# Kernel optimization log

Hardware: AMD Instinct MI355X
Metric: run time of the kernel (lower is better)

The kernel has to match this reference:

```python
import jax, jax.numpy as jnp
import numpy as np
from jax import lax

N, HW = 64, 240
C0, C1, C2, C3 = 3, 32, 64, 128
HEAD = 1280


def _conv(x, w, stride, pad):
    return lax.conv_general_dilated(
        x, w, (stride, stride), [(pad, pad), (pad, pad)],
        dimension_numbers=("NCHW", "OIHW", "NCHW"))


def _cbr(x, w, alpha, beta, stride, pad, do_relu=True):
    # conv2d with pre-folded BN: y = conv(x,w)*alpha + beta, then ReLU
    y = _conv(x, w, stride, pad)
    y = y * alpha[None, :, None, None] + beta[None, :, None, None]
    return jnp.maximum(y, 0.0) if do_relu else y


def setup_inputs() -> dict:
    key = jax.random.key(0)
    ks = jax.random.split(key, 13)
    f32 = jnp.float32
    inp = {
        "x": jax.random.normal(ks[0], (N, C0, HW, HW), dtype=f32),
        # stem 3x3 s2: 3 -> 32
        "w_stem": jax.random.normal(ks[1], (C1, C0, 3, 3), dtype=f32) * 0.1,
        "a_stem": jax.random.uniform(ks[2], (C1,), dtype=f32, minval=0.5, maxval=1.5),
        "b_stem": jax.random.normal(ks[3], (C1,), dtype=f32) * 0.1,
        # mid 3x3 s2: 32 -> 64
        "w1": jax.random.normal(ks[4], (C2, C1, 3, 3), dtype=f32) * 0.05,
        "a1": jax.random.uniform(ks[5], (C2,), dtype=f32, minval=0.5, maxval=1.5),
        "b1": jax.random.normal(ks[6], (C2,), dtype=f32) * 0.1,
        # pointwise 1x1 s1: 64 -> 128
        "w2": jax.random.normal(ks[7], (C3, C2, 1, 1), dtype=f32) * 0.05,
        "a2": jax.random.uniform(ks[8], (C3,), dtype=f32, minval=0.5, maxval=1.5),
        "b2": jax.random.normal(ks[9], (C3,), dtype=f32) * 0.1,
        # head: GAP + GEMV (w2d [Cout, Cin]) + BN-fold + ReLU
        "w_head": jax.random.normal(ks[10], (HEAD, C3), dtype=f32) * 0.05,
        "a_head": jax.random.uniform(ks[11], (HEAD,), dtype=f32, minval=0.5, maxval=1.5),
        "b_head": jax.random.normal(ks[12], (HEAD,), dtype=f32) * 0.1,
    }
    return inp


def reference(x, w_stem, a_stem, b_stem, w1, a1, b1, w2, a2, b2,
              w_head, a_head, b_head):
    h = _cbr(x, w_stem, a_stem, b_stem, stride=2, pad=1)   # [N,32,120,120]
    h = _cbr(h, w1, a1, b1, stride=2, pad=1)               # [N,64,60,60]
    h = _cbr(h, w2, a2, b2, stride=1, pad=0)               # [N,128,60,60]
    # head: global average pool + GEMV + folded-BN affine + ReLU
    gap = h.mean(axis=(2, 3))                              # [N,128]
    out = jnp.einsum("nc,oc->no", gap, w_head)             # [N,1280]
    out = out * a_head[None, :] + b_head[None, :]
    return jnp.maximum(out, 0.0)
```

## Files before the change

### kernel.cpp

```cpp
#include <hip/hip_runtime.h>

#define N_    64
#define HW_   240
#define H1_   120
#define H2_   60
#define C0_   3
#define C1_   32
#define C2_   64
#define C3_   128
#define HEAD_ 1280

typedef unsigned short US;
typedef short bf16x8 __attribute__((ext_vector_type(8)));
typedef float f32x16 __attribute__((ext_vector_type(16)));

__device__ __forceinline__ US f2bf(float f) {
  union { float f; unsigned u; } v; v.f = f;
  unsigned r = v.u + 0x7FFF + ((v.u >> 16) & 1);
  return (US)(r >> 16);
}

#define H1Q_ROW 3968
#define H1Q_PL  1984

__device__ __forceinline__ void gld_lds16(const void* g, void* l) {
  __builtin_amdgcn_global_load_lds(
      (const __attribute__((address_space(1))) unsigned int*)g,
      (__attribute__((address_space(3))) unsigned int*)l, 16, 0, 0);
}

#define ZCHN   368
#define ZTOT   (64 * ZCHN * 4)
__global__ __launch_bounds__(256) void k0_prep(
    const float* __restrict__ w1, const float* __restrict__ w2,
    const float* __restrict__ w0,
    US* __restrict__ h1q, US* __restrict__ wt1, US* __restrict__ wt2,
    US* __restrict__ wt0, float* __restrict__ gap) {
  int gid = blockIdx.x * 256 + threadIdx.x;
  if (gid < ZTOT) {
    int c = gid >> 2, q = gid & 3;
    int n = c / ZCHN, cc = c % ZCHN;
    long off; int y;
    if (cc < 124)      { y = 0;   off = (long)cc * 32; }
    else if (cc < 248) { y = 121; off = (long)(cc - 124) * 32; }
    else               { y = cc - 247; off = H1Q_PL; }
    uint4 z; z.x = z.y = z.z = z.w = 0u;
    *(uint4*)(h1q + ((long)(n * 122 + y)) * H1Q_ROW + off + q * 8) = z;
  } else if (gid < ZTOT + 18432) {
    int e = gid - ZTOT;
    int oc = e / 288, ic = (e / 9) % 32, ky = (e / 3) % 3, kx = e % 3;
    wt1[((ky * 3 + kx) * 64 + oc) * 32 + ic] = f2bf(w1[e]);
  } else if (gid < ZTOT + 18432 + 8192) {
    int e = gid - (ZTOT + 18432);
    wt2[e] = f2bf(w2[e]);
  } else if (gid < ZTOT + 18432 + 8192 + 1024) {
    int e = gid - (ZTOT + 18432 + 8192);
    int oc = e >> 5, k = e & 31;
    wt0[e] = (k < 27) ? f2bf(w0[oc * 27 + k]) : (US)0;
  } else if (gid < ZTOT + 18432 + 8192 + 1024 + 8192) {
    gap[gid - (ZTOT + 18432 + 8192 + 1024)] = 0.f;
  }
}

#define XSW 248
__global__ __launch_bounds__(256) void k1_mfma(
    const float* __restrict__ x, const US* __restrict__ wt0,
    const float* __restrict__ alpha, const float* __restrict__ beta,
    US* __restrict__ h1q) {
  __shared__ __align__(16) float xs[3 * 3 * XSW];
  __shared__ US ot[128 * 32];
  int y = blockIdx.x, n = blockIdx.y;
  int iy0 = 2 * y - 1;
  const float* xn = x + (long)n * C0_ * HW_ * HW_;
  int t = threadIdx.x, w = t >> 6, l = t & 63;

  if (t < 18) {
    int seg = t >> 1, end = t & 1;
    float4 z; z.x = z.y = z.z = z.w = 0.f;
    *(float4*)(xs + seg * XSW + (end ? 244 : 0)) = z;
  }
  if (y == 0) {
    float4 z; z.x = z.y = z.z = z.w = 0.f;
    for (int e = t; e < 180; e += 256) {
      int m = e % 60, icz = e / 60;
      *(float4*)(xs + (icz * 3) * XSW + 4 + 4 * m) = z;
    }
  }
  __syncthreads();

  for (int sgi = w; sgi < 9; sgi += 4) {
    int ic = sgi / 3, r = sgi - (sgi / 3) * 3;
    int iy = iy0 + r;
    if (iy >= 0 && l < 60)
      gld_lds16((const char*)(xn + (long)ic * HW_ * HW_ + (long)iy * HW_) +
                    l * 16,
                (char*)(xs + sgi * XSW + 4) + l * 16);
  }
  __syncthreads();

  int wv = w;
  int lane31 = l & 31, half = l >> 5;
  int ox = wv * 32 + lane31;
  int oxc = ox < H1_ ? ox : (H1_ - 1);

  float fa[16];
#pragma unroll
  for (int m = 0; m < 2; m++)
#pragma unroll
    for (int j = 0; j < 8; j++) {
      int k = m * 16 + half * 8 + j;
      float v = 0.f;
      if (k < 27) {
        int ic = k / 9, rem = k - ic * 9;
        int ky = rem / 3, kx = rem - ky * 3;
        v = xs[(ic * 3 + ky) * XSW + 3 + 2 * oxc + kx];
      }
      fa[m * 8 + j] = v;
    }
  bf16x8 a0, a1;
#pragma unroll
  for (int j = 0; j < 8; j++) {
    a0[j] = (short)f2bf(fa[j]);
    a1[j] = (short)f2bf(fa[8 + j]);
  }
  const US* wb = wt0 + lane31 * 32 + half * 8;
  bf16x8 b0 = *(const bf16x8*)(wb);
  bf16x8 b1 = *(const bf16x8*)(wb + 16);

  f32x16 acc;
#pragma unroll
  for (int i = 0; i < 16; i++) acc[i] = 0.f;
  acc = __builtin_amdgcn_mfma_f32_32x32x16_bf16(a0, b0, acc, 0, 0, 0);
  acc = __builtin_amdgcn_mfma_f32_32x32x16_bf16(a1, b1, acc, 0, 0, 0);

  int oc = lane31;
  float al = alpha[oc], be = beta[oc];
#pragma unroll
  for (int r = 0; r < 16; r++) {
    int row = (r & 3) + 8 * (r >> 2) + 4 * half;
    float v = fmaxf(fmaf(acc[r], al, be), 0.f);
    ot[(wv * 32 + row) * 32 + oc] = f2bf(v);
  }
  __syncthreads();

  long rowb = ((long)(n * 122 + y + 1)) * H1Q_ROW;
  for (int u = t; u < 480; u += 256) {
    int px = u >> 2, q = u & 3;
    int pl = px & 1;
    int m = (px + 1) >> 1;
    long addr = rowb + (pl ? H1Q_PL : 0) + (long)m * 32 + q * 8;
    *(uint4*)(h1q + addr) = *(const uint4*)(ot + px * 32 + q * 8);
  }
}

#define TS 72
__global__ __launch_bounds__(256, 2) void k2_fused(
    const US* __restrict__ h1q, const US* __restrict__ wt1,
    const US* __restrict__ wt2,
    const float* __restrict__ a1, const float* __restrict__ b1,
    const float* __restrict__ a2, const float* __restrict__ b2,
    float* __restrict__ gap) {
  __shared__ __align__(16) US st[6 * 4096];
  __shared__ __align__(16) US tile[64 * TS];
  int t = threadIdx.x, w = t >> 6, l = t & 63;
  int lane31 = l & 31, half = l >> 5;

  int n = 8 * blockIdx.x + (blockIdx.y & 7);
  int bxr = blockIdx.y >> 3;
  int ny = bxr < 4 ? 8 : 7;
  int y0 = bxr < 4 ? bxr * 8 : 32 + (bxr - 4) * 7;

  const char* nb = (const char*)(h1q + (long)(n * 122) * H1Q_ROW);

  int wm = w & 1, wn = w >> 1;
  int oc = wn * 32 + lane31;
  int pt = w & 1, og = w >> 1;
  bf16x8 wA[9][2];
#pragma unroll
  for (int kk = 0; kk < 9; kk++)
#pragma unroll
    for (int c = 0; c < 2; c++)
      wA[kk][c] = *(const bf16x8*)(wt1 + (kk * 64 + oc) * 32 + half * 8 + c * 16);
  bf16x8 wB[2][4];
  float al2[2], be2[2];
#pragma unroll
  for (int nt = 0; nt < 2; nt++) {
    int oc2 = (og * 2 + nt) * 32 + lane31;
#pragma unroll
    for (int c = 0; c < 4; c++)
      wB[nt][c] = *(const bf16x8*)(wt2 + oc2 * 64 + half * 8 + c * 16);
    al2[nt] = a2[oc2]; be2[nt] = b2[oc2];
  }
  float al1 = a1[oc], be1 = b1[oc];

  int px = wm * 32 + lane31;
  int xx = px < 60 ? px : 59;
  int abase = xx * 32 + half * 8;
  int usofs[3][2];
#pragma unroll
  for (int kx = 0; kx < 3; kx++)
#pragma unroll
    for (int c = 0; c < 2; c++) {
      int uo = (kx == 1 ? 0 : (kx == 0 ? 1984 : 2016)) + abase + c * 16;
      usofs[kx][c] = uo ^ (((uo >> 6) & 7) << 3);
    }

#pragma unroll
  for (int i = 0; i < 6; i++) {
    int c = i * 256 + t;
    int rw = c >> 9;
    int b = (c & 511) * 16;
    int sb = b ^ (((b >> 7) & 7) << 4);
    int r = 2 * y0 + rw;
    gld_lds16(nb + (long)r * 7936 + sb, (char*)st + (r % 6) * 8192 + b);
  }
  __syncthreads();

  for (int iy = 0; iy < ny; iy++) {
    int y = y0 + iy;
    if (iy + 1 < ny) {
#pragma unroll
      for (int i = 0; i < 4; i++) {
        int c = i * 256 + t;
        int rw = c >> 9;
        int b = (c & 511) * 16;
        int sb = b ^ (((b >> 7) & 7) << 4);
        int r = 2 * y + 3 + rw;
        gld_lds16(nb + (long)r * 7936 + sb,
                  (char*)st + (r % 6) * 8192 + b);
      }
    }

    f32x16 acc;
#pragma unroll
    for (int i = 0; i < 16; i++) acc[i] = 0.f;
#pragma unroll
    for (int ky = 0; ky < 3; ky++) {
      int r = 2 * y + ky;
      int sb6 = (r % 6) * 4096;
#pragma unroll
      for (int kx = 0; kx < 3; kx++) {
#pragma unroll
        for (int c = 0; c < 2; c++) {
          bf16x8 av = *(const bf16x8*)(st + sb6 + usofs[kx][c]);
          acc = __builtin_amdgcn_mfma_f32_32x32x16_bf16(av, wA[ky * 3 + kx][c],
                                                        acc, 0, 0, 0);
        }
      }
    }
#pragma unroll
    for (int r = 0; r < 16; r++) {
      int row = (r & 3) + 8 * (r >> 2) + 4 * half;
      tile[(wm * 32 + row) * TS + oc] = f2bf(fmaxf(fmaf(acc[r], al1, be1), 0.f));
    }
    __syncthreads();

    const US* ab = tile + (pt * 32 + lane31) * TS + half * 8;
    bf16x8 af[4];
#pragma unroll
    for (int c = 0; c < 4; c++) af[c] = *(const bf16x8*)(ab + c * 16);

#pragma unroll
    for (int nt = 0; nt < 2; nt++) {
      int oc2 = (og * 2 + nt) * 32 + lane31;
      f32x16 acc2;
#pragma unroll
      for (int i = 0; i < 16; i++) acc2[i] = 0.f;
#pragma unroll
      for (int c = 0; c < 4; c++)
        acc2 = __builtin_amdgcn_mfma_f32_32x32x16_bf16(af[c], wB[nt][c], acc2,
                                                       0, 0, 0);
      float s = 0.f;
      if (pt == 0) {
#pragma unroll
        for (int r = 0; r < 16; r++) s += fmaxf(fmaf(acc2[r], al2[nt], be2[nt]), 0.f);
      } else {
#pragma unroll
        for (int r = 0; r < 16; r++) {
          int row = (r & 3) + 8 * (r >> 2) + 4 * half;
          if (32 + row < 60) s += fmaxf(fmaf(acc2[r], al2[nt], be2[nt]), 0.f);
        }
      }
      s += __shfl_xor(s, 32);
      if (half == 0) atomicAdd(gap + n * C3_ + oc2, s);
    }
    __syncthreads();
  }
}

__global__ __launch_bounds__(256) void k4_head(
    const float* __restrict__ gap, const float* __restrict__ wh,
    const float* __restrict__ alpha, const float* __restrict__ beta,
    float* __restrict__ out) {
  __shared__ float g[8 * C3_];
  int n0 = blockIdx.y * 8;
  int t = threadIdx.x;
  for (int e = t; e < 8 * C3_; e += 256)
    g[e] = gap[n0 * C3_ + e] * (1.f / 3600.f);
  __syncthreads();
  int o = blockIdx.x * 256 + t;
  const float* wr = wh + (long)o * C3_;
  float acc[8];
#pragma unroll
  for (int i = 0; i < 8; i++) acc[i] = 0.f;
#pragma unroll 4
  for (int c = 0; c < C3_; c += 4) {
    float4 wv = *(const float4*)(wr + c);
#pragma unroll
    for (int i = 0; i < 8; i++) {
      const float* gi = g + i * C3_ + c;
      acc[i] = fmaf(wv.x, gi[0], acc[i]);
      acc[i] = fmaf(wv.y, gi[1], acc[i]);
      acc[i] = fmaf(wv.z, gi[2], acc[i]);
      acc[i] = fmaf(wv.w, gi[3], acc[i]);
    }
  }
  float al = alpha[o], be = beta[o];
#pragma unroll
  for (int i = 0; i < 8; i++)
    out[(n0 + i) * HEAD_ + o] = fmaxf(fmaf(acc[i], al, be), 0.f);
}

extern "C" void kernel_launch(void* const* d_in, const int* in_sizes, int n_in,
                              void* d_out, int out_size, void* d_ws,
                              size_t ws_size, hipStream_t stream) {
  const float* x      = (const float*)d_in[0];
  const float* w_stem = (const float*)d_in[1];
  const float* a_stem = (const float*)d_in[2];
  const float* b_stem = (const float*)d_in[3];
  const float* w1     = (const float*)d_in[4];
  const float* a1     = (const float*)d_in[5];
  const float* b1     = (const float*)d_in[6];
  const float* w2     = (const float*)d_in[7];
  const float* a2     = (const float*)d_in[8];
  const float* b2     = (const float*)d_in[9];
  const float* wh     = (const float*)d_in[10];
  const float* ah     = (const float*)d_in[11];
  const float* bh     = (const float*)d_in[12];
  float* out = (float*)d_out;

  US* h1q = (US*)d_ws;
  US* wt1 = h1q + (size_t)N_ * 122 * H1Q_ROW;
  US* wt2 = wt1 + 9 * 64 * 32;
  US* wt0 = wt2 + C3_ * C2_;
  float* gap = (float*)(wt0 + 1024);

  {
    int total = ZTOT + 18432 + 8192 + 1024 + 8192;
    k0_prep<<<(total + 255) / 256, 256, 0, stream>>>(w1, w2, w_stem, h1q,
                                                     wt1, wt2, wt0, gap);
  }
  {
    dim3 grid(H1_, N_);
    k1_mfma<<<grid, 256, 0, stream>>>(x, wt0, a_stem, b_stem, h1q);
  }
  {
    dim3 grid(8, N_);
    k2_fused<<<grid, 256, 0, stream>>>(h1q, wt1, wt2, a1, b1, a2, b2, gap);
  }
  {
    dim3 grid(HEAD_ / 256, 8);
    k4_head<<<grid, 256, 0, stream>>>(gap, wh, ah, bh, out);
  }
}
```

Measured before the change: 148.7 us.

## Compute two stem rows per block and retile fused conv into 5-row strips

The stem kernel now stages 5 input rows per channel and produces two output rows per block. This halves the grid and cuts the redundant re-reading of overlapping input rows. The fused mid/pointwise kernel splits each image into 12 strips of 5 output rows instead of 8 uneven strips. It shrinks the LDS ring buffer from 6 to 5 rows and raises the launch-bounds occupancy hint to 3 blocks per CU. The trade-off is more register and LDS pressure per stem block, and more per-block weight loading overhead in the fused kernel, in exchange for better parallelism and occupancy.

```diff
diff --git a/kernel.cpp b/kernel.cpp
--- a/kernel.cpp
+++ b/kernel.cpp
@@ -67,30 +67,30 @@
     const float* __restrict__ x, const US* __restrict__ wt0,
     const float* __restrict__ alpha, const float* __restrict__ beta,
     US* __restrict__ h1q) {
-  __shared__ __align__(16) float xs[3 * 3 * XSW];
-  __shared__ US ot[128 * 32];
-  int y = blockIdx.x, n = blockIdx.y;
-  int iy0 = 2 * y - 1;
+  __shared__ __align__(16) float xs[15 * XSW];
+  __shared__ US ot[256 * 32];
+  int Y = blockIdx.x, n = blockIdx.y;
+  int iyb = 4 * Y - 1;
   const float* xn = x + (long)n * C0_ * HW_ * HW_;
   int t = threadIdx.x, w = t >> 6, l = t & 63;
 
-  if (t < 18) {
+  if (t < 30) {
     int seg = t >> 1, end = t & 1;
     float4 z; z.x = z.y = z.z = z.w = 0.f;
     *(float4*)(xs + seg * XSW + (end ? 244 : 0)) = z;
   }
-  if (y == 0) {
+  if (Y == 0) {
     float4 z; z.x = z.y = z.z = z.w = 0.f;
     for (int e = t; e < 180; e += 256) {
       int m = e % 60, icz = e / 60;
-      *(float4*)(xs + (icz * 3) * XSW + 4 + 4 * m) = z;
-    }
-  }
-  __syncthreads();
-
-  for (int sgi = w; sgi < 9; sgi += 4) {
-    int ic = sgi / 3, r = sgi - (sgi / 3) * 3;
-    int iy = iy0 + r;
+      *(float4*)(xs + (icz * 5) * XSW + 4 + 4 * m) = z;
+    }
+  }
+  __syncthreads();
+
+  for (int sgi = w; sgi < 15; sgi += 4) {
+    int ic = sgi / 5, r5 = sgi - (sgi / 5) * 5;
+    int iy = iyb + r5;
     if (iy >= 0 && l < 60)
       gld_lds16((const char*)(xn + (long)ic * HW_ * HW_ + (long)iy * HW_) +
                     l * 16,
@@ -98,77 +98,77 @@
   }
   __syncthreads();
 
-  int wv = w;
   int lane31 = l & 31, half = l >> 5;
-  int ox = wv * 32 + lane31;
-  int oxc = ox < H1_ ? ox : (H1_ - 1);
-
-  float fa[16];
-#pragma unroll
-  for (int m = 0; m < 2; m++)
-#pragma unroll
-    for (int j = 0; j < 8; j++) {
-      int k = m * 16 + half * 8 + j;
-      float v = 0.f;
-      if (k < 27) {
-        int ic = k / 9, rem = k - ic * 9;
-        int ky = rem / 3, kx = rem - ky * 3;
-        v = xs[(ic * 3 + ky) * XSW + 3 + 2 * oxc + kx];
-      }
-      fa[m * 8 + j] = v;
-    }
-  bf16x8 a0, a1;
-#pragma unroll
-  for (int j = 0; j < 8; j++) {
-    a0[j] = (short)f2bf(fa[j]);
-    a1[j] = (short)f2bf(fa[8 + j]);
-  }
   const US* wb = wt0 + lane31 * 32 + half * 8;
   bf16x8 b0 = *(const bf16x8*)(wb);
   bf16x8 b1 = *(const bf16x8*)(wb + 16);
-
-  f32x16 acc;
-#pragma unroll
-  for (int i = 0; i < 16; i++) acc[i] = 0.f;
-  acc = __builtin_amdgcn_mfma_f32_32x32x16_bf16(a0, b0, acc, 0, 0, 0);
-  acc = __builtin_amdgcn_mfma_f32_32x32x16_bf16(a1, b1, acc, 0, 0, 0);
-
   int oc = lane31;
   float al = alpha[oc], be = beta[oc];
-#pragma unroll
-  for (int r = 0; r < 16; r++) {
-    int row = (r & 3) + 8 * (r >> 2) + 4 * half;
-    float v = fmaxf(fmaf(acc[r], al, be), 0.f);
-    ot[(wv * 32 + row) * 32 + oc] = f2bf(v);
-  }
-  __syncthreads();
-
-  long rowb = ((long)(n * 122 + y + 1)) * H1Q_ROW;
-  for (int u = t; u < 480; u += 256) {
-    int px = u >> 2, q = u & 3;
+
+#pragma unroll
+  for (int rowsel = 0; rowsel < 2; rowsel++) {
+    int ox = w * 32 + lane31;
+    int oxc = ox < H1_ ? ox : (H1_ - 1);
+    float fa[16];
+#pragma unroll
+    for (int m = 0; m < 2; m++)
+#pragma unroll
+      for (int j = 0; j < 8; j++) {
+        int k = m * 16 + half * 8 + j;
+        float v = 0.f;
+        if (k < 27) {
+          int ic = k / 9, rem = k - ic * 9;
+          int ky = rem / 3, kx = rem - ky * 3;
+          v = xs[(ic * 5 + 2 * rowsel + ky) * XSW + 3 + 2 * oxc + kx];
+        }
+        fa[m * 8 + j] = v;
+      }
+    bf16x8 a0, a1;
+#pragma unroll
+    for (int j = 0; j < 8; j++) {
+      a0[j] = (short)f2bf(fa[j]);
+      a1[j] = (short)f2bf(fa[8 + j]);
+    }
+    f32x16 acc;
+#pragma unroll
+    for (int i = 0; i < 16; i++) acc[i] = 0.f;
+    acc = __builtin_amdgcn_mfma_f32_32x32x16_bf16(a0, b0, acc, 0, 0, 0);
+    acc = __builtin_amdgcn_mfma_f32_32x32x16_bf16(a1, b1, acc, 0, 0, 0);
+#pragma unroll
+    for (int r = 0; r < 16; r++) {
+      int row = (r & 3) + 8 * (r >> 2) + 4 * half;
+      float v = fmaxf(fmaf(acc[r], al, be), 0.f);
+      ot[(rowsel * 128 + w * 32 + row) * 32 + oc] = f2bf(v);
+    }
+  }
+  __syncthreads();
+
+  for (int u = t; u < 960; u += 256) {
+    int rowsel = u / 480, uu = u - rowsel * 480;
+    int px = uu >> 2, q = uu & 3;
     int pl = px & 1;
     int m = (px + 1) >> 1;
+    long rowb = ((long)(n * 122 + 2 * Y + rowsel + 1)) * H1Q_ROW;
     long addr = rowb + (pl ? H1Q_PL : 0) + (long)m * 32 + q * 8;
-    *(uint4*)(h1q + addr) = *(const uint4*)(ot + px * 32 + q * 8);
+    *(uint4*)(h1q + addr) = *(const uint4*)(ot + (rowsel * 128 + px) * 32 + q * 8);
   }
 }
 
 #define TS 72
-__global__ __launch_bounds__(256, 2) void k2_fused(
+__global__ __launch_bounds__(256, 3) void k2_fused(
     const US* __restrict__ h1q, const US* __restrict__ wt1,
     const US* __restrict__ wt2,
     const float* __restrict__ a1, const float* __restrict__ b1,
     const float* __restrict__ a2, const float* __restrict__ b2,
     float* __restrict__ gap) {
-  __shared__ __align__(16) US st[6 * 4096];
+  __shared__ __align__(16) US st[5 * 4096];
   __shared__ __align__(16) US tile[64 * TS];
   int t = threadIdx.x, w = t >> 6, l = t & 63;
   int lane31 = l & 31, half = l >> 5;
 
   int n = 8 * blockIdx.x + (blockIdx.y & 7);
   int bxr = blockIdx.y >> 3;
-  int ny = bxr < 4 ? 8 : 7;
-  int y0 = bxr < 4 ? bxr * 8 : 32 + (bxr - 4) * 7;
+  int y0 = bxr * 5;
 
   const char* nb = (const char*)(h1q + (long)(n * 122) * H1Q_ROW);
 
@@ -212,13 +212,13 @@
     int b = (c & 511) * 16;
     int sb = b ^ (((b >> 7) & 7) << 4);
     int r = 2 * y0 + rw;
-    gld_lds16(nb + (long)r * 7936 + sb, (char*)st + (r % 6) * 8192 + b);
-  }
-  __syncthreads();
-
-  for (int iy = 0; iy < ny; iy++) {
+    gld_lds16(nb + (long)r * 7936 + sb, (char*)st + (r % 5) * 8192 + b);
+  }
+  __syncthreads();
+
+  for (int iy = 0; iy < 5; iy++) {
     int y = y0 + iy;
-    if (iy + 1 < ny) {
+    if (iy < 4) {
 #pragma unroll
       for (int i = 0; i < 4; i++) {
         int c = i * 256 + t;
@@ -227,7 +227,7 @@
         int sb = b ^ (((b >> 7) & 7) << 4);
         int r = 2 * y + 3 + rw;
         gld_lds16(nb + (long)r * 7936 + sb,
-                  (char*)st + (r % 6) * 8192 + b);
+                  (char*)st + (r % 5) * 8192 + b);
       }
     }
 
@@ -237,12 +237,12 @@
 #pragma unroll
     for (int ky = 0; ky < 3; ky++) {
       int r = 2 * y + ky;
-      int sb6 = (r % 6) * 4096;
+      int sb5 = (r % 5) * 4096;
 #pragma unroll
       for (int kx = 0; kx < 3; kx++) {
 #pragma unroll
         for (int c = 0; c < 2; c++) {
-          bf16x8 av = *(const bf16x8*)(st + sb6 + usofs[kx][c]);
+          bf16x8 av = *(const bf16x8*)(st + sb5 + usofs[kx][c]);
           acc = __builtin_amdgcn_mfma_f32_32x32x16_bf16(av, wA[ky * 3 + kx][c],
                                                         acc, 0, 0, 0);
         }
@@ -351,11 +351,11 @@
                                                      wt1, wt2, wt0, gap);
   }
   {
-    dim3 grid(H1_, N_);
+    dim3 grid(H2_, N_);
     k1_mfma<<<grid, 256, 0, stream>>>(x, wt0, a_stem, b_stem, h1q);
   }
   {
-    dim3 grid(8, N_);
+    dim3 grid(8, 96);
     k2_fused<<<grid, 256, 0, stream>>>(h1q, wt1, wt2, a1, b1, a2, b2, gap);
   }
   {
```

Measured after the change: 150.9 us. No clear change (+1.5%).

## Deepen k2 row ring to prefetch two rows ahead with fine-grained waits

Applied to the files above, without the earlier changes.

Grows the LDS row ring from 6 to 8 slots so the fused conv kernel prefetches input rows two output rows ahead instead of one. __syncthreads is replaced by explicit vmcnt/lgkmcnt waits plus s_barrier, so outstanding prefetches no longer stall each iteration. Per-row atomics into the GAP buffer become per-thread partial sums with one atomicAdd at the end. The extra 16 KB of LDS may lower occupancy below two blocks per CU, and the hand-counted vmcnt values must match the number of outstanding loads.

```diff
diff --git a/kernel.cpp b/kernel.cpp
--- a/kernel.cpp
+++ b/kernel.cpp
@@ -160,7 +160,7 @@
     const float* __restrict__ a1, const float* __restrict__ b1,
     const float* __restrict__ a2, const float* __restrict__ b2,
     float* __restrict__ gap) {
-  __shared__ __align__(16) US st[6 * 4096];
+  __shared__ __align__(16) US st[8 * 4096];
   __shared__ __align__(16) US tile[64 * TS];
   int t = threadIdx.x, w = t >> 6, l = t & 63;
   int lane31 = l & 31, half = l >> 5;
@@ -192,6 +192,7 @@
     al2[nt] = a2[oc2]; be2[nt] = b2[oc2];
   }
   float al1 = a1[oc], be1 = b1[oc];
+  float gsum[2] = {0.f, 0.f};
 
   int px = wm * 32 + lane31;
   int xx = px < 60 ? px : 59;
@@ -206,28 +207,29 @@
     }
 
 #pragma unroll
-  for (int i = 0; i < 6; i++) {
+  for (int i = 0; i < 10; i++) {
     int c = i * 256 + t;
     int rw = c >> 9;
     int b = (c & 511) * 16;
     int sb = b ^ (((b >> 7) & 7) << 4);
     int r = 2 * y0 + rw;
-    gld_lds16(nb + (long)r * 7936 + sb, (char*)st + (r % 6) * 8192 + b);
-  }
-  __syncthreads();
+    gld_lds16(nb + (long)r * 7936 + sb, (char*)st + (r & 7) * 8192 + b);
+  }
+  asm volatile("s_waitcnt vmcnt(0)" ::: "memory");
+  __builtin_amdgcn_s_barrier();
+  __builtin_amdgcn_sched_barrier(0);
 
   for (int iy = 0; iy < ny; iy++) {
     int y = y0 + iy;
-    if (iy + 1 < ny) {
+    if (iy + 2 < ny) {
 #pragma unroll
       for (int i = 0; i < 4; i++) {
         int c = i * 256 + t;
         int rw = c >> 9;
         int b = (c & 511) * 16;
         int sb = b ^ (((b >> 7) & 7) << 4);
-        int r = 2 * y + 3 + rw;
-        gld_lds16(nb + (long)r * 7936 + sb,
-                  (char*)st + (r % 6) * 8192 + b);
+        int r = 2 * y + 5 + rw;
+        gld_lds16(nb + (long)r * 7936 + sb, (char*)st + (r & 7) * 8192 + b);
       }
     }
 
@@ -237,12 +239,12 @@
 #pragma unroll
     for (int ky = 0; ky < 3; ky++) {
       int r = 2 * y + ky;
-      int sb6 = (r % 6) * 4096;
+      int sb8 = (r & 7) * 4096;
 #pragma unroll
       for (int kx = 0; kx < 3; kx++) {
 #pragma unroll
         for (int c = 0; c < 2; c++) {
-          bf16x8 av = *(const bf16x8*)(st + sb6 + usofs[kx][c]);
+          bf16x8 av = *(const bf16x8*)(st + sb8 + usofs[kx][c]);
           acc = __builtin_amdgcn_mfma_f32_32x32x16_bf16(av, wA[ky * 3 + kx][c],
                                                         acc, 0, 0, 0);
         }
@@ -253,7 +255,9 @@
       int row = (r & 3) + 8 * (r >> 2) + 4 * half;
       tile[(wm * 32 + row) * TS + oc] = f2bf(fmaxf(fmaf(acc[r], al1, be1), 0.f));
     }
-    __syncthreads();
+    asm volatile("s_waitcnt lgkmcnt(0)" ::: "memory");
+    __builtin_amdgcn_s_barrier();
+    __builtin_amdgcn_sched_barrier(0);
 
     const US* ab = tile + (pt * 32 + lane31) * TS + half * 8;
     bf16x8 af[4];
@@ -262,7 +266,6 @@
 
 #pragma unroll
     for (int nt = 0; nt < 2; nt++) {
-      int oc2 = (og * 2 + nt) * 32 + lane31;
       f32x16 acc2;
 #pragma unroll
       for (int i = 0; i < 16; i++) acc2[i] = 0.f;
@@ -281,10 +284,27 @@
           if (32 + row < 60) s += fmaxf(fmaf(acc2[r], al2[nt], be2[nt]), 0.f);
         }
       }
-      s += __shfl_xor(s, 32);
-      if (half == 0) atomicAdd(gap + n * C3_ + oc2, s);
-    }
-    __syncthreads();
+      gsum[nt] += s;
+    }
+
+    if (iy + 1 < ny) {
+      if (iy + 2 < ny)
+        asm volatile("s_waitcnt vmcnt(4) lgkmcnt(0)" ::: "memory");
+      else
+        asm volatile("s_waitcnt vmcnt(0) lgkmcnt(0)" ::: "memory");
+      __builtin_amdgcn_s_barrier();
+      __builtin_amdgcn_sched_barrier(0);
+    }
+  }
+
+#pragma unroll
+  for (int nt = 0; nt < 2; nt++) {
+    float s = gsum[nt];
+    s += __shfl_xor(s, 32);
+    if (half == 0) {
+      int oc2 = (og * 2 + nt) * 32 + lane31;
+      atomicAdd(gap + n * C3_ + oc2, s);
+    }
   }
 }
 
```

Measured after the change: 150.8 us. No clear change (+1.4%).
